# Performance work log

Measured on AMD Instinct MI355X. Metric: run time of the kernel, lower is better.

The kernel has to match this reference:

```python
import jax, jax.numpy as jnp
import numpy as np
from math import sqrt

N = 400000
MUL0, MUL1 = 64, 32            # multiplicities of 0e and 1o in irreps_in1 / irreps_out
DIM_IN1 = MUL0 + 3 * MUL1      # 160 = e3nn layout [64x0e | 32x1o]

# UnnormalisedFullyConnectedTensorProduct path coefficients:
# path_weight = mul1*mul2*n_paths_to_out, irrep_normalization='component',
# path_normalization='path' => coeff = sqrt(ir_out.dim / (mul1*mul2*n_paths_to_out)).
# Each output irrep (0e and 1o) receives exactly 2 paths here.
C_SS0 = sqrt(1.0 / (MUL0 * 1 * 2))   # 0e x 0e -> 0e
C_VV0 = sqrt(1.0 / (MUL1 * 1 * 2))   # 1o x 1o -> 0e
C_SV1 = sqrt(3.0 / (MUL0 * 1 * 2))   # 0e x 1o -> 1o
C_VS1 = sqrt(3.0 / (MUL1 * 1 * 2))   # 1o x 0e -> 1o
INV_SQRT3 = 1.0 / sqrt(3.0)          # real-basis wigner_3j values for the l=1 paths


def setup_inputs() -> dict:
    key = jax.random.key(0)
    ks = jax.random.split(key, 7)
    return {
        "x1": jax.random.normal(ks[0], (N, DIM_IN1), jnp.float32),
        "x2": jax.random.normal(ks[1], (N, 4), jnp.float32),   # 1x0e + 1x1o attribute
        # uvw weights, one [mul1, mul2, mul_out] block per CG path
        "W_ss0": jax.random.normal(ks[2], (MUL0, 1, MUL0), jnp.float32) * 0.05,
        "W_vv0": jax.random.normal(ks[3], (MUL1, 1, MUL0), jnp.float32) * 0.05,
        "W_sv1": jax.random.normal(ks[4], (MUL0, 1, MUL1), jnp.float32) * 0.05,
        "W_vs1": jax.random.normal(ks[5], (MUL1, 1, MUL1), jnp.float32) * 0.05,
        # bias only for the scalar (0e) output slice
        "bias0": jax.random.normal(ks[6], (MUL0,), jnp.float32) * 0.05,
    }


def reference(x1, x2, W_ss0, W_vv0, W_sv1, W_vs1, bias0):
    # split e3nn-layout inputs into irrep blocks
    s1 = x1[:, :MUL0]                      # [N, 64]     0e block
    v1 = x1[:, MUL0:].reshape(-1, MUL1, 3) # [N, 32, 3]  1o block (mul-major)
    s2 = x2[:, :1]                         # [N, 1]
    v2 = x2[:, 1:].reshape(-1, 1, 3)       # [N, 1, 3]

    # scalar output: 0e x 0e -> 0e  (w3j = [[[1]]])
    out0 = C_SS0 * jnp.einsum('uvw,bu,bv->bw', W_ss0, s1, s2)
    # scalar output: 1o x 1o -> 0e  (w3j[i,j,0] = delta_ij / sqrt(3))
    out0 = out0 + (C_VV0 * INV_SQRT3) * jnp.einsum('uvw,bui,bvi->bw', W_vv0, v1, v2)
    # slice-wise bias add on l=0 channels
    out0 = out0 + bias0

    # vector output: 0e x 1o -> 1o  (w3j[0,j,k] = delta_jk / sqrt(3))
    out1 = (C_SV1 * INV_SQRT3) * jnp.einsum('uvw,bu,bvk->bwk', W_sv1, s1, v2)
    # vector output: 1o x 0e -> 1o  (w3j[i,0,k] = delta_ik / sqrt(3))
    out1 = out1 + (C_VS1 * INV_SQRT3) * jnp.einsum('uvw,bui,bv->bwi', W_vs1, v1, s2)

    return jnp.concatenate([out0, out1.reshape(-1, MUL1 * 3)], axis=-1)  # [N, 160]
```

## Files before the change

kernel.cpp:

```cpp
#include <hip/hip_runtime.h>

typedef __bf16 bf16x8 __attribute__((ext_vector_type(8)));
typedef float floatx4 __attribute__((ext_vector_type(4)));

static constexpr int ROW_IN  = 160;
static constexpr int ROW_OUT = 160;

static constexpr float C_SS0_F    = 0.08838834764831845f;
static constexpr float C_VV0_I3_F = 0.07216878364870323f;
static constexpr float C_SV1_I3_F = 0.08838834764831845f;
static constexpr float C_VS1_I3_F = 0.125f;

__device__ __forceinline__ floatx4 mfma16(bf16x8 a, bf16x8 b, floatx4 c) {
    return __builtin_amdgcn_mfma_f32_16x16x32_bf16(a, b, c, 0, 0, 0);
}

__global__ __launch_bounds__(256, 2)
void o3tp_kernel(const float* __restrict__ x1, const float* __restrict__ x2,
                 const float* __restrict__ Wss0, const float* __restrict__ Wvv0,
                 const float* __restrict__ Wsv1, const float* __restrict__ Wvs1,
                 const float* __restrict__ bias0, float* __restrict__ out, int n)
{
    const int lane = threadIdx.x & 63;
    const int m = lane & 15;
    const int q = lane >> 4;

    bf16x8 Bss[2][4];
    bf16x8 Bvv[4];
    bf16x8 Bsv[2][2];
    bf16x8 Bvs[2];
#pragma unroll
    for (int kt = 0; kt < 2; ++kt)
#pragma unroll
        for (int ct = 0; ct < 4; ++ct)
#pragma unroll
            for (int j = 0; j < 8; ++j)
                Bss[kt][ct][j] = (__bf16)Wss0[(kt*32 + q*8 + j)*64 + ct*16 + m];
#pragma unroll
    for (int ct = 0; ct < 4; ++ct)
#pragma unroll
        for (int j = 0; j < 8; ++j)
            Bvv[ct][j] = (__bf16)Wvv0[(q*8 + j)*64 + ct*16 + m];
#pragma unroll
    for (int kt = 0; kt < 2; ++kt)
#pragma unroll
        for (int ct = 0; ct < 2; ++ct)
#pragma unroll
            for (int j = 0; j < 8; ++j)
                Bsv[kt][ct][j] = (__bf16)(Wsv1[(kt*32 + q*8 + j)*32 + ct*16 + m] * C_SV1_I3_F);
#pragma unroll
    for (int ct = 0; ct < 2; ++ct)
#pragma unroll
        for (int j = 0; j < 8; ++j)
            Bvs[ct][j] = (__bf16)Wvs1[(q*8 + j)*32 + ct*16 + m];

    float bias_r[4];
#pragma unroll
    for (int ct = 0; ct < 4; ++ct) bias_r[ct] = bias0[ct*16 + m];

    const floatx4 zero = {0.f, 0.f, 0.f, 0.f};

    const int n_tiles = n >> 4;
    const int wid     = blockIdx.x * (blockDim.x >> 6) + (threadIdx.x >> 6);
    const int n_waves = gridDim.x * (blockDim.x >> 6);

    for (int tile = wid; tile < n_tiles; tile += n_waves) {
        const int row0 = tile << 4;
        const float* __restrict__ xr = x1 + (size_t)(row0 + m) * ROW_IN;
        const float4 x2m = *(const float4*)(x2 + (size_t)(row0 + m) * 4);

        bf16x8 a_s[2], a_ss[2];
        const float sscale = x2m.x * C_SS0_F;
#pragma unroll
        for (int kt = 0; kt < 2; ++kt) {
            const float4 f0 = *(const float4*)(xr + kt*32 + q*8);
            const float4 f1 = *(const float4*)(xr + kt*32 + q*8 + 4);
            const float v[8] = {f0.x, f0.y, f0.z, f0.w, f1.x, f1.y, f1.z, f1.w};
#pragma unroll
            for (int j = 0; j < 8; ++j) {
                a_s[kt][j]  = (__bf16)v[j];
                a_ss[kt][j] = (__bf16)(v[j] * sscale);
            }
        }

        float c[24];
#pragma unroll
        for (int t = 0; t < 6; ++t) {
            const float4 f = *(const float4*)(xr + 64 + q*24 + t*4);
            c[t*4+0] = f.x; c[t*4+1] = f.y; c[t*4+2] = f.z; c[t*4+3] = f.w;
        }
        bf16x8 a_d, a_v0, a_v1, a_v2;
        const float gscale = x2m.x * C_VS1_I3_F;
#pragma unroll
        for (int j = 0; j < 8; ++j) {
            const float d = (c[3*j+0]*x2m.y + c[3*j+1]*x2m.z + c[3*j+2]*x2m.w) * C_VV0_I3_F;
            a_d[j]  = (__bf16)d;
            a_v0[j] = (__bf16)(c[3*j+0] * gscale);
            a_v1[j] = (__bf16)(c[3*j+1] * gscale);
            a_v2[j] = (__bf16)(c[3*j+2] * gscale);
        }

        floatx4 acc0[4], accT[2], accG[3][2];
#pragma unroll
        for (int ct = 0; ct < 4; ++ct) {
            acc0[ct] = mfma16(a_ss[0], Bss[0][ct], zero);
            acc0[ct] = mfma16(a_ss[1], Bss[1][ct], acc0[ct]);
            acc0[ct] = mfma16(a_d,     Bvv[ct],    acc0[ct]);
        }
#pragma unroll
        for (int ct = 0; ct < 2; ++ct) {
            accT[ct] = mfma16(a_s[0], Bsv[0][ct], zero);
            accT[ct] = mfma16(a_s[1], Bsv[1][ct], accT[ct]);
            accG[0][ct] = mfma16(a_v0, Bvs[ct], zero);
            accG[1][ct] = mfma16(a_v1, Bvs[ct], zero);
            accG[2][ct] = mfma16(a_v2, Bvs[ct], zero);
        }

#pragma unroll
        for (int r = 0; r < 4; ++r) {
            const int row = row0 + q*4 + r;
            float* __restrict__ orow = out + (size_t)row * ROW_OUT;
            const float4 x2r = *(const float4*)(x2 + (size_t)row * 4);
#pragma unroll
            for (int ct = 0; ct < 4; ++ct)
                orow[ct*16 + m] = acc0[ct][r] + bias_r[ct];
#pragma unroll
            for (int ct = 0; ct < 2; ++ct) {
                const int w = ct*16 + m;
                const float t = accT[ct][r];
                orow[64 + 3*w + 0] = x2r.y * t + accG[0][ct][r];
                orow[64 + 3*w + 1] = x2r.z * t + accG[1][ct][r];
                orow[64 + 3*w + 2] = x2r.w * t + accG[2][ct][r];
            }
        }
    }
}

extern "C" void kernel_launch(void* const* d_in, const int* in_sizes, int n_in,
                              void* d_out, int out_size, void* d_ws, size_t ws_size,
                              hipStream_t stream) {
    const float* x1    = (const float*)d_in[0];
    const float* x2    = (const float*)d_in[1];
    const float* Wss0  = (const float*)d_in[2];
    const float* Wvv0  = (const float*)d_in[3];
    const float* Wsv1  = (const float*)d_in[4];
    const float* Wvs1  = (const float*)d_in[5];
    const float* bias0 = (const float*)d_in[6];
    float* out = (float*)d_out;
    const int n = in_sizes[0] / ROW_IN;

    dim3 grid(512), block(256);
    hipLaunchKernelGGL(o3tp_kernel, grid, block, 0, stream,
                       x1, x2, Wss0, Wvv0, Wsv1, Wvs1, bias0, out, n);
}
```

Baseline: 436.5 us.

## Stage input and output tiles through per-wave LDS for coalesced global access

Each wave now loads its 16-row x1 tile with fully coalesced float4 reads into a padded per-wave LDS buffer, then reads MFMA operands from LDS. Results are written to the same LDS buffer and streamed out with coalesced float4 stores, replacing scattered per-row scalar global stores. The per-row x2 reload is replaced by lane shuffles. This adds LDS traffic and wave-level waits, and relies on intra-wave ordering without barriers.

```diff
diff --git a/kernel.cpp b/kernel.cpp
--- a/kernel.cpp
+++ b/kernel.cpp
@@ -5,6 +5,7 @@
 
 static constexpr int ROW_IN  = 160;
 static constexpr int ROW_OUT = 160;
+static constexpr int LDS_STRIDE = 164;
 
 static constexpr float C_SS0_F    = 0.08838834764831845f;
 static constexpr float C_VV0_I3_F = 0.07216878364870323f;
@@ -21,6 +22,9 @@
                  const float* __restrict__ Wsv1, const float* __restrict__ Wvs1,
                  const float* __restrict__ bias0, float* __restrict__ out, int n)
 {
+    __shared__ float lds[4][16 * LDS_STRIDE];
+    float* __restrict__ tl = lds[threadIdx.x >> 6];
+
     const int lane = threadIdx.x & 63;
     const int m = lane & 15;
     const int q = lane >> 4;
@@ -66,23 +70,37 @@
 
     for (int tile = wid; tile < n_tiles; tile += n_waves) {
         const int row0 = tile << 4;
-        const float* __restrict__ xr = x1 + (size_t)(row0 + m) * ROW_IN;
+
+        asm volatile("" ::: "memory");
+        const float* __restrict__ src = x1 + (size_t)row0 * ROW_IN;
+        float4 v[10];
+#pragma unroll
+        for (int it = 0; it < 10; ++it)
+            v[it] = *(const float4*)(src + (it*64 + lane)*4);
         const float4 x2m = *(const float4*)(x2 + (size_t)(row0 + m) * 4);
+#pragma unroll
+        for (int it = 0; it < 10; ++it) {
+            const int f   = it*64 + lane;
+            const int row = f / 40;
+            const int col = f*4 - row*ROW_IN;
+            *(float4*)(tl + row*LDS_STRIDE + col) = v[it];
+        }
+        asm volatile("s_waitcnt lgkmcnt(0)" ::: "memory");
 
+        const float* __restrict__ xr = tl + m * LDS_STRIDE;
         bf16x8 a_s[2], a_ss[2];
         const float sscale = x2m.x * C_SS0_F;
 #pragma unroll
         for (int kt = 0; kt < 2; ++kt) {
             const float4 f0 = *(const float4*)(xr + kt*32 + q*8);
             const float4 f1 = *(const float4*)(xr + kt*32 + q*8 + 4);
-            const float v[8] = {f0.x, f0.y, f0.z, f0.w, f1.x, f1.y, f1.z, f1.w};
+            const float vv[8] = {f0.x, f0.y, f0.z, f0.w, f1.x, f1.y, f1.z, f1.w};
 #pragma unroll
             for (int j = 0; j < 8; ++j) {
-                a_s[kt][j]  = (__bf16)v[j];
-                a_ss[kt][j] = (__bf16)(v[j] * sscale);
+                a_s[kt][j]  = (__bf16)vv[j];
+                a_ss[kt][j] = (__bf16)(vv[j] * sscale);
             }
         }
-
         float c[24];
 #pragma unroll
         for (int t = 0; t < 6; ++t) {
@@ -116,11 +134,14 @@
             accG[2][ct] = mfma16(a_v2, Bvs[ct], zero);
         }
 
+        asm volatile("" ::: "memory");
 #pragma unroll
         for (int r = 0; r < 4; ++r) {
-            const int row = row0 + q*4 + r;
-            float* __restrict__ orow = out + (size_t)row * ROW_OUT;
-            const float4 x2r = *(const float4*)(x2 + (size_t)row * 4);
+            const int rr = q*4 + r;
+            const float xy = __shfl(x2m.y, rr, 64);
+            const float xz = __shfl(x2m.z, rr, 64);
+            const float xw = __shfl(x2m.w, rr, 64);
+            float* __restrict__ orow = tl + rr * LDS_STRIDE;
 #pragma unroll
             for (int ct = 0; ct < 4; ++ct)
                 orow[ct*16 + m] = acc0[ct][r] + bias_r[ct];
@@ -128,10 +149,21 @@
             for (int ct = 0; ct < 2; ++ct) {
                 const int w = ct*16 + m;
                 const float t = accT[ct][r];
-                orow[64 + 3*w + 0] = x2r.y * t + accG[0][ct][r];
-                orow[64 + 3*w + 1] = x2r.z * t + accG[1][ct][r];
-                orow[64 + 3*w + 2] = x2r.w * t + accG[2][ct][r];
+                orow[64 + 3*w + 0] = xy * t + accG[0][ct][r];
+                orow[64 + 3*w + 1] = xz * t + accG[1][ct][r];
+                orow[64 + 3*w + 2] = xw * t + accG[2][ct][r];
             }
+        }
+        asm volatile("s_waitcnt lgkmcnt(0)" ::: "memory");
+
+        float* __restrict__ dst = out + (size_t)row0 * ROW_OUT;
+#pragma unroll
+        for (int it = 0; it < 10; ++it) {
+            const int f   = it*64 + lane;
+            const int row = f / 40;
+            const int col = f*4 - row*ROW_OUT;
+            const float4 vv = *(const float4*)(tl + row*LDS_STRIDE + col);
+            *(float4*)(dst + f*4) = vv;
         }
     }
 }
```

Result: no change. 435.7 us (-0.2%).
